# Performance work log

Measured on AMD Instinct MI355X. Metric: run time of the kernel, lower is better.

The kernel has to match this reference:

```python
import jax, jax.numpy as jnp
import numpy as np

D_MODEL = 512
NHEAD = 8
HEAD_DIM = D_MODEL // NHEAD


def setup_inputs() -> dict:
    key = jax.random.key(0)
    ks = jax.random.split(key, 12)
    B, T = 2, 4096
    inp = {
        'query': jax.random.normal(ks[0], (B, T, D_MODEL), jnp.float32),
        'key': jax.random.normal(ks[1], (B, T, D_MODEL), jnp.float32),
        'value': jax.random.normal(ks[2], (B, T, D_MODEL), jnp.float32),
        'frac': jax.random.uniform(ks[3], (B, T), jnp.float32),
        # learned parameters (torch nn.Linear: y = x @ W.T + b)
        'Wq': jax.random.normal(ks[4], (D_MODEL, D_MODEL), jnp.float32) * (D_MODEL ** -0.5),
        'bq': jnp.zeros((D_MODEL,), jnp.float32),
        'Wk': jax.random.normal(ks[5], (D_MODEL, D_MODEL), jnp.float32) * (D_MODEL ** -0.5),
        'bk': jnp.zeros((D_MODEL,), jnp.float32),
        'Wv': jax.random.normal(ks[6], (D_MODEL, D_MODEL), jnp.float32) * (D_MODEL ** -0.5),
        'bv': jnp.zeros((D_MODEL,), jnp.float32),
        'Wo': jax.random.normal(ks[7], (D_MODEL, D_MODEL), jnp.float32) * (D_MODEL ** -0.5),
        'bo': jnp.zeros((D_MODEL,), jnp.float32),
        'alpha_pos': jax.random.normal(ks[8], (NHEAD,), jnp.float32) * 0.1,
        'alpha_neg': jax.random.normal(ks[9], (NHEAD,), jnp.float32) * 0.1,
    }
    return inp


def reference(query, key, value, frac, Wq, bq, Wk, bk, Wv, bv, Wo, bo, alpha_pos, alpha_neg):
    B, T, _ = query.shape
    scale = HEAD_DIM ** -0.5
    # projections (torch Linear convention: x @ W.T + b)
    Q = (query @ Wq.T + bq).reshape(B, T, NHEAD, HEAD_DIM).transpose(0, 2, 1, 3)
    K = (key @ Wk.T + bk).reshape(B, T, NHEAD, HEAD_DIM).transpose(0, 2, 1, 3)
    V = (value @ Wv.T + bv).reshape(B, T, NHEAD, HEAD_DIM).transpose(0, 2, 1, 3)
    scores = jnp.einsum('bhqd,bhkd->bhqk', Q, K) * scale  # [B,H,T,T]
    # stoichiometric bias: D[b,i,j] = frac[b,j] - frac[b,i]
    D = frac[:, None, :] - frac[:, :, None]  # [B,T,T]
    D_pos = jnp.maximum(D, 0.0)
    D_neg = jnp.minimum(D, 0.0)
    bias = (alpha_pos[None, :, None, None] * D_pos[:, None]
            + alpha_neg[None, :, None, None] * D_neg[:, None])  # [B,H,T,T]
    probs = jax.nn.softmax(scores + bias, axis=-1)
    out = jnp.einsum('bhqk,bhkd->bhqd', probs, V)
    out = out.transpose(0, 2, 1, 3).reshape(B, T, D_MODEL)
    return out @ Wo.T + bo
```

## Files before the change

### kernel.cpp

```cpp
#include <hip/hip_runtime.h>

typedef __attribute__((ext_vector_type(8))) __bf16 bf16x8;
typedef __attribute__((ext_vector_type(8))) unsigned short ushort8;
typedef __attribute__((ext_vector_type(4))) float f32x4;
typedef unsigned short ushort_t;

#define MFMA_BF16(A,B,C) __builtin_amdgcn_mfma_f32_16x16x32_bf16(A,B,C,0,0,0)

#define T_SEQ 4096
#define DM 512
#define HD_ 64
#define NH_ 8

#define LOG2E 1.4426950408889634f
#define QSCALE (0.125f * LOG2E)

__device__ __forceinline__ unsigned short f2b(float f){
    unsigned int u = __builtin_bit_cast(unsigned int, f);
    u += 0x7FFFu + ((u >> 16) & 1u);
    return (unsigned short)(u >> 16);
}

__device__ __forceinline__ float exp2_fast(float x){
#if __has_builtin(__builtin_amdgcn_exp2f)
    return __builtin_amdgcn_exp2f(x);
#else
    float r; asm("v_exp_f32 %0, %1" : "=v"(r) : "v"(x)); return r;
#endif
}

__device__ __forceinline__ unsigned cvt_pk_bf16(float a, float b){
    unsigned r;
    asm("v_cvt_pk_bf16_f32 %0, %1, %2" : "=v"(r) : "v"(a), "v"(b));
    return r;
}

__device__ __forceinline__ void gload_lds16(const void* g, void* l){
    __builtin_amdgcn_global_load_lds((const __attribute__((address_space(1))) void*)g,
                                     (__attribute__((address_space(3))) void*)l, 16, 0, 0);
}

template<int OUT_BF16>
__device__ __forceinline__ void gemm_body(const float* __restrict__ A, const float* __restrict__ W,
                                          const float* __restrict__ bias, void* __restrict__ Cout,
                                          int m0, int n0, float scale)
{
    constexpr int K = 512, N = 512;
    __shared__ ushort_t As[128*64];
    __shared__ ushort_t Bs[128*64];

    const int tid  = threadIdx.x;
    const int lane = tid & 63;
    const int w    = tid >> 6;
    const int g    = lane >> 4;
    const int c16  = lane & 15;
    const int wm   = w >> 1, wn = w & 1;

    f32x4 acc[4][4];
#pragma unroll
    for (int i=0;i<4;i++)
#pragma unroll
        for (int j=0;j<4;j++) acc[i][j] = (f32x4){0.f,0.f,0.f,0.f};

#pragma unroll 1
    for (int kt=0; kt<K/64; kt++){
        __syncthreads();
#pragma unroll
        for (int j=0;j<4;j++){
            int cid = j*256 + tid;
            int row = cid >> 3, ch = cid & 7;
            const float* srcA = A + (size_t)(m0+row)*K + kt*64 + ch*8;
            const float* srcB = W + (size_t)(n0+row)*K + kt*64 + ch*8;
            float4 a0 = *(const float4*)srcA;
            float4 a1 = *(const float4*)(srcA+4);
            float4 b0 = *(const float4*)srcB;
            float4 b1 = *(const float4*)(srcB+4);
            ushort8 va, vb;
            va[0]=f2b(a0.x); va[1]=f2b(a0.y); va[2]=f2b(a0.z); va[3]=f2b(a0.w);
            va[4]=f2b(a1.x); va[5]=f2b(a1.y); va[6]=f2b(a1.z); va[7]=f2b(a1.w);
            vb[0]=f2b(b0.x); vb[1]=f2b(b0.y); vb[2]=f2b(b0.z); vb[3]=f2b(b0.w);
            vb[4]=f2b(b1.x); vb[5]=f2b(b1.y); vb[6]=f2b(b1.z); vb[7]=f2b(b1.w);
            int dst = row*64 + ((ch ^ (row & 7))<<3);
            *(ushort8*)&As[dst] = va;
            *(ushort8*)&Bs[dst] = vb;
        }
        __syncthreads();
#pragma unroll
        for (int ks=0; ks<2; ks++){
            bf16x8 af[4], bfr[4];
#pragma unroll
            for (int f=0; f<4; f++){
                int rowa = wm*64 + f*16 + c16;
                af[f]  = *(const bf16x8*)&As[rowa*64 + (((ks*4+g) ^ (rowa&7))<<3)];
                int rowb = wn*64 + f*16 + c16;
                bfr[f] = *(const bf16x8*)&Bs[rowb*64 + (((ks*4+g) ^ (rowb&7))<<3)];
            }
#pragma unroll
            for (int fm=0; fm<4; fm++)
#pragma unroll
                for (int fn=0; fn<4; fn++)
                    acc[fm][fn] = MFMA_BF16(af[fm], bfr[fn], acc[fm][fn]);
        }
    }
#pragma unroll
    for (int fm=0; fm<4; fm++)
#pragma unroll
        for (int fn=0; fn<4; fn++){
            int col = n0 + wn*64 + fn*16 + c16;
            float bv = bias[col];
#pragma unroll
            for (int r=0; r<4; r++){
                int rowm = m0 + wm*64 + fm*16 + g*4 + r;
                float vv = (acc[fm][fn][r] + bv) * scale;
                if (OUT_BF16) ((ushort_t*)Cout)[(size_t)rowm*N + col] = f2b(vv);
                else          ((float*)Cout)[(size_t)rowm*N + col]   = vv;
            }
        }
}

__global__ __launch_bounds__(256,2) void gemm_qkv_kernel(
    const float* __restrict__ q, const float* __restrict__ k, const float* __restrict__ v,
    const float* __restrict__ Wq, const float* __restrict__ bq,
    const float* __restrict__ Wk, const float* __restrict__ bk,
    const float* __restrict__ Wv, const float* __restrict__ bv,
    ushort_t* __restrict__ QKVp)
{
    int z = blockIdx.z;
    const float* A  = (z==0) ? q  : (z==1 ? k  : v);
    const float* W  = (z==0) ? Wq : (z==1 ? Wk : Wv);
    const float* bb = (z==0) ? bq : (z==1 ? bk : bv);
    float scale = (z==0) ? QSCALE : 1.0f;
    ushort_t* C = QKVp + (size_t)z * (size_t)(2*T_SEQ) * DM;
    gemm_body<1>(A, W, bb, C, blockIdx.x*128, blockIdx.y*128, scale);
}

__global__ __launch_bounds__(256,2) void gemm_out_kernel(
    const float* __restrict__ O, const float* __restrict__ Wo,
    const float* __restrict__ bo, float* __restrict__ out)
{
    gemm_body<0>(O, Wo, bo, out, blockIdx.x*128, blockIdx.y*128, 1.0f);
}

__global__ __launch_bounds__(256) void vtrans_kernel(const ushort_t* __restrict__ Vp,
                                                     ushort_t* __restrict__ Vt)
{
    int blk = blockIdx.x;
    int bh  = blk >> 6;
    int t0  = (blk & 63) << 6;
    int b = bh >> 3, h = bh & 7;
    __shared__ ushort_t tile[64][65];
    const int tid = threadIdx.x;
    const ushort_t* src = Vp + (size_t)(b*T_SEQ + t0)*DM + h*HD_;
#pragma unroll
    for (int p=0; p<2; p++){
        int row = (tid>>3) + p*32;
        int c8  = (tid&7)*8;
        ushort8 v = *(const ushort8*)(src + (size_t)row*DM + c8);
#pragma unroll
        for (int j=0;j<8;j++) tile[row][c8+j] = v[j];
    }
    __syncthreads();
    ushort_t* dst = Vt + (size_t)bh*HD_*T_SEQ + t0;
#pragma unroll
    for (int p=0; p<2; p++){
        int d  = (tid>>3) + p*32;
        int c8 = (tid&7)*8;
        ushort8 v;
#pragma unroll
        for (int j=0;j<8;j++) v[j] = tile[c8+j][d];
        *(ushort8*)(dst + (size_t)d*T_SEQ + c8) = v;
    }
}

__global__ __launch_bounds__(512,4) void flash_kernel(
    const ushort_t* __restrict__ Qp, const ushort_t* __restrict__ Kp, const ushort_t* __restrict__ Vt,
    const float* __restrict__ frac, const float* __restrict__ alphap, const float* __restrict__ alphan,
    float* __restrict__ O)
{
    int i    = blockIdx.x;
    int slot = i & 7;
    int seq  = i >> 3;
    int bh   = slot*2 + (seq >> 5);
    int qt   = seq & 31;
    int b    = bh >> 3, h = bh & 7;
    int q0   = qt * 128;

    const int tid  = threadIdx.x;
    const int w    = tid >> 6;
    const int lane = tid & 63;
    const int g    = lane >> 4;
    const int c16  = lane & 15;

    __shared__ ushort_t Ks [2][64*64];
    __shared__ ushort_t VTs[2][64*64];
    __shared__ ushort_t PW [8][16*64];

    const ushort_t* Qbase = Qp + (size_t)(b*T_SEQ)*DM + h*HD_;
    const ushort_t* Kbase = Kp + (size_t)(b*T_SEQ)*DM + h*HD_;
    const ushort_t* Vtb   = Vt + (size_t)bh*HD_*T_SEQ;
    const float*    fr    = frac + b*T_SEQ;
    const float c1 = 0.5f*(alphap[h] + alphan[h]) * LOG2E;
    const float c2 = 0.5f*(alphap[h] - alphan[h]) * LOG2E;
    const int qrow = q0 + w*16;

    bf16x8 qa[2];
#pragma unroll
    for (int ks=0; ks<2; ks++)
        qa[ks] = *(const bf16x8*)(Qbase + (size_t)(qrow + c16)*DM + ks*32 + g*8);
    const float fi = fr[qrow + c16];

    float m2   = -1e30f;
    float lsum = 0.f;
    f32x4 acc[4];
#pragma unroll
    for (int dt=0; dt<4; dt++) acc[dt] = (f32x4){0.f,0.f,0.f,0.f};

    bf16x8 vbp[2][4];

#define STAGE(BUF, KV0)                                                          \
    {                                                                            \
        int cb  = w*64;                                                          \
        int idx = cb + lane;                                                     \
        int row = idx >> 3, cc = idx & 7;                                        \
        int cs  = cc ^ (row & 7);                                                \
        gload_lds16(Kbase + (size_t)((KV0)+row)*DM + cs*8, &Ks[BUF][cb*8]);      \
        gload_lds16(Vtb + (size_t)row*T_SEQ + (KV0) + cs*8, &VTs[BUF][cb*8]);    \
    }

    STAGE(0, 0);
    asm volatile("s_waitcnt vmcnt(0)" ::: "memory");
    __syncthreads();

    int buf = 0;
#pragma unroll 1
    for (int kt=0; kt<T_SEQ/64; kt++){
        int kv0 = kt*64;
        if (kt+1 < T_SEQ/64) STAGE(buf^1, kv0+64);

        bf16x8 pb0, pb1;
        if (kt > 0){
            pb0 = *(const bf16x8*)&PW[w][c16*64 + (((    g) ^ (c16&7))<<3)];
            pb1 = *(const bf16x8*)&PW[w][c16*64 + (((4 + g) ^ (c16&7))<<3)];
        }

        f32x4 s[4];
#pragma unroll
        for (int n=0; n<4; n++) s[n] = (f32x4){0.f,0.f,0.f,0.f};
        __builtin_amdgcn_s_setprio(1);
#pragma unroll
        for (int n=0; n<4; n++){
#pragma unroll
            for (int ks=0; ks<2; ks++){
                int row = n*16 + c16;
                bf16x8 kb = *(const bf16x8*)&Ks[buf][row*64 + (((ks*4+g) ^ (row&7))<<3)];
                s[n] = MFMA_BF16(kb, qa[ks], s[n]);
            }
        }
        if (kt > 0){
#pragma unroll
            for (int dt=0; dt<4; dt++) acc[dt] = MFMA_BF16(vbp[0][dt], pb0, acc[dt]);
#pragma unroll
            for (int dt=0; dt<4; dt++) acc[dt] = MFMA_BF16(vbp[1][dt], pb1, acc[dt]);
        }
        __builtin_amdgcn_s_setprio(0);
        __builtin_amdgcn_sched_barrier(0);

        float mx;
#pragma unroll
        for (int n=0; n<4; n++){
            f32x4 fj = *(const f32x4*)&fr[kv0 + n*16 + g*4];
#pragma unroll
            for (int r=0; r<4; r++){
                float dd = fj[r] - fi;
                s[n][r] = fmaf(c1, dd, fmaf(c2, fabsf(dd), s[n][r]));
            }
            float t = fmaxf(fmaxf(s[n][0], s[n][1]), fmaxf(s[n][2], s[n][3]));
            mx = (n==0) ? t : fmaxf(mx, t);
        }
        mx = fmaxf(mx, __shfl_xor(mx, 16));
        mx = fmaxf(mx, __shfl_xor(mx, 32));

        if (__any(mx > m2 + 12.0f)){
            float mnew = fmaxf(m2, mx);
            float fac  = exp2_fast(m2 - mnew);
            lsum *= fac;
#pragma unroll
            for (int dt=0; dt<4; dt++)
#pragma unroll
                for (int r=0; r<4; r++) acc[dt][r] *= fac;
            m2 = mnew;
        }

        float tn[4];
#pragma unroll
        for (int n=0; n<4; n++){
#pragma unroll
            for (int r=0; r<4; r++) s[n][r] = exp2_fast(s[n][r] - m2);
            tn[n] = (s[n][0] + s[n][1]) + (s[n][2] + s[n][3]);
            unsigned pk0 = cvt_pk_bf16(s[n][0], s[n][1]);
            unsigned pk1 = cvt_pk_bf16(s[n][2], s[n][3]);
            uint2 u; u.x = pk0; u.y = pk1;
            int off = c16*64 + (((n*2 + (g>>1)) ^ (c16 & 7))<<3) + ((g&1)<<2);
            *(uint2*)&PW[w][off] = u;
        }
        float rs = (tn[0] + tn[1]) + (tn[2] + tn[3]);
        rs += __shfl_xor(rs, 16);
        rs += __shfl_xor(rs, 32);
        lsum += rs;

#pragma unroll
        for (int ks=0; ks<2; ks++)
#pragma unroll
            for (int dt=0; dt<4; dt++){
                int vr = dt*16 + c16;
                vbp[ks][dt] = *(const bf16x8*)&VTs[buf][vr*64 + (((ks*4+g) ^ (vr&7))<<3)];
            }

        asm volatile("s_waitcnt vmcnt(0)" ::: "memory");
        __syncthreads();
        buf ^= 1;
    }
#undef STAGE

    {
        bf16x8 pb0 = *(const bf16x8*)&PW[w][c16*64 + (((    g) ^ (c16&7))<<3)];
        bf16x8 pb1 = *(const bf16x8*)&PW[w][c16*64 + (((4 + g) ^ (c16&7))<<3)];
#pragma unroll
        for (int dt=0; dt<4; dt++) acc[dt] = MFMA_BF16(vbp[0][dt], pb0, acc[dt]);
#pragma unroll
        for (int dt=0; dt<4; dt++) acc[dt] = MFMA_BF16(vbp[1][dt], pb1, acc[dt]);
    }

    float inv = 1.0f / lsum;
    float* orow = O + (size_t)(b*T_SEQ + qrow + c16)*DM + h*HD_;
#pragma unroll
    for (int dt=0; dt<4; dt++){
        float4 o4;
        o4.x = acc[dt][0]*inv; o4.y = acc[dt][1]*inv;
        o4.z = acc[dt][2]*inv; o4.w = acc[dt][3]*inv;
        *(float4*)(orow + dt*16 + g*4) = o4;
    }
}

extern "C" void kernel_launch(void* const* d_in, const int* in_sizes, int n_in,
                              void* d_out, int out_size, void* d_ws, size_t ws_size,
                              hipStream_t stream)
{
    const float* q  = (const float*)d_in[0];
    const float* k  = (const float*)d_in[1];
    const float* v  = (const float*)d_in[2];
    const float* fr = (const float*)d_in[3];
    const float* Wq = (const float*)d_in[4];
    const float* bq = (const float*)d_in[5];
    const float* Wk = (const float*)d_in[6];
    const float* bk = (const float*)d_in[7];
    const float* Wv = (const float*)d_in[8];
    const float* bv = (const float*)d_in[9];
    const float* Wo = (const float*)d_in[10];
    const float* bo = (const float*)d_in[11];
    const float* ap = (const float*)d_in[12];
    const float* an = (const float*)d_in[13];

    const size_t MT = (size_t)(2*T_SEQ) * DM;
    ushort_t* QKVp = (ushort_t*)d_ws;
    ushort_t* Vtp  = QKVp + 3*MT;
    float*    O    = (float*)((char*)d_ws + 4*MT*sizeof(ushort_t));

    dim3 gq(64, 4, 3);
    gemm_qkv_kernel<<<gq, 256, 0, stream>>>(q,k,v,Wq,bq,Wk,bk,Wv,bv,QKVp);

    vtrans_kernel<<<1024, 256, 0, stream>>>(QKVp + 2*MT, Vtp);

    flash_kernel<<<512, 512, 0, stream>>>(QKVp, QKVp + MT, Vtp, fr, ap, an, O);

    dim3 go(64, 4, 1);
    gemm_out_kernel<<<go, 256, 0, stream>>>(O, Wo, bo, (float*)d_out);
}
```

Measured before the change: 171.6 us.

## Fuse V transpose into QKV GEMM epilogue and compute row sums via MFMA

The V projection GEMM now writes its output directly in the head-major transposed layout, which removes the separate transpose kernel launch and its extra global read and write of V. Inside the flash kernel, the softmax row sum is accumulated with an extra MFMA against a vector of bf16 ones, replacing the VALU additions and cross-lane shuffle reduction. The row max is computed with a flatter tree of three-input max operations. The trade-offs are uncoalesced 8-byte scattered stores in the V epilogue and a row sum built from bf16-rounded probabilities, which can differ slightly from the fp32 sum.

```diff
diff --git a/kernel.cpp b/kernel.cpp
--- a/kernel.cpp
+++ b/kernel.cpp
@@ -2,6 +2,7 @@
 
 typedef __attribute__((ext_vector_type(8))) __bf16 bf16x8;
 typedef __attribute__((ext_vector_type(8))) unsigned short ushort8;
+typedef __attribute__((ext_vector_type(4))) unsigned short ushort4_t;
 typedef __attribute__((ext_vector_type(4))) float f32x4;
 typedef unsigned short ushort_t;
 
@@ -29,6 +30,10 @@
 #endif
 }
 
+__device__ __forceinline__ float max3f(float a, float b, float c){
+    return fmaxf(fmaxf(a, b), c);
+}
+
 __device__ __forceinline__ unsigned cvt_pk_bf16(float a, float b){
     unsigned r;
     asm("v_cvt_pk_bf16_f32 %0, %1, %2" : "=v"(r) : "v"(a), "v"(b));
@@ -40,7 +45,7 @@
                                      (__attribute__((address_space(3))) void*)l, 16, 0, 0);
 }
 
-template<int OUT_BF16>
+template<int MODE>
 __device__ __forceinline__ void gemm_body(const float* __restrict__ A, const float* __restrict__ W,
                                           const float* __restrict__ bias, void* __restrict__ Cout,
                                           int m0, int n0, float scale)
@@ -108,12 +113,24 @@
         for (int fn=0; fn<4; fn++){
             int col = n0 + wn*64 + fn*16 + c16;
             float bv = bias[col];
-#pragma unroll
-            for (int r=0; r<4; r++){
-                int rowm = m0 + wm*64 + fm*16 + g*4 + r;
-                float vv = (acc[fm][fn][r] + bv) * scale;
-                if (OUT_BF16) ((ushort_t*)Cout)[(size_t)rowm*N + col] = f2b(vv);
-                else          ((float*)Cout)[(size_t)rowm*N + col]   = vv;
+            if (MODE == 2){
+                int t0r = m0 + wm*64 + fm*16 + g*4;
+                int b2  = t0r >> 12;
+                int t   = t0r & 4095;
+                int h2  = col >> 6, d = col & 63;
+                ushort4_t u;
+#pragma unroll
+                for (int r=0; r<4; r++) u[r] = f2b(acc[fm][fn][r] + bv);
+                ushort_t* dst = (ushort_t*)Cout + ((size_t)(b2*NH_ + h2)*HD_ + d)*T_SEQ + t;
+                *(ushort4_t*)dst = u;
+            } else {
+#pragma unroll
+                for (int r=0; r<4; r++){
+                    int rowm = m0 + wm*64 + fm*16 + g*4 + r;
+                    float vv = (acc[fm][fn][r] + bv) * scale;
+                    if (MODE == 1) ((ushort_t*)Cout)[(size_t)rowm*N + col] = f2b(vv);
+                    else           ((float*)Cout)[(size_t)rowm*N + col]   = vv;
+                }
             }
         }
 }
@@ -129,9 +146,12 @@
     const float* A  = (z==0) ? q  : (z==1 ? k  : v);
     const float* W  = (z==0) ? Wq : (z==1 ? Wk : Wv);
     const float* bb = (z==0) ? bq : (z==1 ? bk : bv);
-    float scale = (z==0) ? QSCALE : 1.0f;
     ushort_t* C = QKVp + (size_t)z * (size_t)(2*T_SEQ) * DM;
-    gemm_body<1>(A, W, bb, C, blockIdx.x*128, blockIdx.y*128, scale);
+    if (z == 2)
+        gemm_body<2>(A, W, bb, C, blockIdx.x*128, blockIdx.y*128, 1.0f);
+    else
+        gemm_body<1>(A, W, bb, C, blockIdx.x*128, blockIdx.y*128,
+                     (z==0) ? QSCALE : 1.0f);
 }
 
 __global__ __launch_bounds__(256,2) void gemm_out_kernel(
@@ -139,37 +159,6 @@
     const float* __restrict__ bo, float* __restrict__ out)
 {
     gemm_body<0>(O, Wo, bo, out, blockIdx.x*128, blockIdx.y*128, 1.0f);
-}
-
-__global__ __launch_bounds__(256) void vtrans_kernel(const ushort_t* __restrict__ Vp,
-                                                     ushort_t* __restrict__ Vt)
-{
-    int blk = blockIdx.x;
-    int bh  = blk >> 6;
-    int t0  = (blk & 63) << 6;
-    int b = bh >> 3, h = bh & 7;
-    __shared__ ushort_t tile[64][65];
-    const int tid = threadIdx.x;
-    const ushort_t* src = Vp + (size_t)(b*T_SEQ + t0)*DM + h*HD_;
-#pragma unroll
-    for (int p=0; p<2; p++){
-        int row = (tid>>3) + p*32;
-        int c8  = (tid&7)*8;
-        ushort8 v = *(const ushort8*)(src + (size_t)row*DM + c8);
-#pragma unroll
-        for (int j=0;j<8;j++) tile[row][c8+j] = v[j];
-    }
-    __syncthreads();
-    ushort_t* dst = Vt + (size_t)bh*HD_*T_SEQ + t0;
-#pragma unroll
-    for (int p=0; p<2; p++){
-        int d  = (tid>>3) + p*32;
-        int c8 = (tid&7)*8;
-        ushort8 v;
-#pragma unroll
-        for (int j=0;j<8;j++) v[j] = tile[c8+j][d];
-        *(ushort8*)(dst + (size_t)d*T_SEQ + c8) = v;
-    }
 }
 
 __global__ __launch_bounds__(512,4) void flash_kernel(
@@ -209,11 +198,17 @@
         qa[ks] = *(const bf16x8*)(Qbase + (size_t)(qrow + c16)*DM + ks*32 + g*8);
     const float fi = fr[qrow + c16];
 
-    float m2   = -1e30f;
-    float lsum = 0.f;
+    ushort8 ou;
+#pragma unroll
+    for (int j=0;j<8;j++) ou[j] = 0x3F80;
+    const bf16x8 ones = __builtin_bit_cast(bf16x8, ou);
+
+    float m2 = -1e30f;
     f32x4 acc[4];
+    f32x4 asum;
 #pragma unroll
     for (int dt=0; dt<4; dt++) acc[dt] = (f32x4){0.f,0.f,0.f,0.f};
+    asum = (f32x4){0.f,0.f,0.f,0.f};
 
     bf16x8 vbp[2][4];
 
@@ -257,15 +252,16 @@
             }
         }
         if (kt > 0){
+            asum = MFMA_BF16(ones, pb0, asum);
 #pragma unroll
             for (int dt=0; dt<4; dt++) acc[dt] = MFMA_BF16(vbp[0][dt], pb0, acc[dt]);
+            asum = MFMA_BF16(ones, pb1, asum);
 #pragma unroll
             for (int dt=0; dt<4; dt++) acc[dt] = MFMA_BF16(vbp[1][dt], pb1, acc[dt]);
         }
         __builtin_amdgcn_s_setprio(0);
         __builtin_amdgcn_sched_barrier(0);
 
-        float mx;
 #pragma unroll
         for (int n=0; n<4; n++){
             f32x4 fj = *(const f32x4*)&fr[kv0 + n*16 + g*4];
@@ -274,8 +270,15 @@
                 float dd = fj[r] - fi;
                 s[n][r] = fmaf(c1, dd, fmaf(c2, fabsf(dd), s[n][r]));
             }
-            float t = fmaxf(fmaxf(s[n][0], s[n][1]), fmaxf(s[n][2], s[n][3]));
-            mx = (n==0) ? t : fmaxf(mx, t);
+        }
+        float mx;
+        {
+            float t0 = max3f(s[0][0], s[0][1], s[0][2]);
+            float t1 = max3f(s[0][3], s[1][0], s[1][1]);
+            float t2 = max3f(s[1][2], s[1][3], s[2][0]);
+            float t3 = max3f(s[2][1], s[2][2], s[2][3]);
+            float t4 = max3f(s[3][0], s[3][1], s[3][2]);
+            mx = fmaxf(max3f(t0, t1, t2), max3f(t3, t4, s[3][3]));
         }
         mx = fmaxf(mx, __shfl_xor(mx, 16));
         mx = fmaxf(mx, __shfl_xor(mx, 32));
@@ -283,7 +286,8 @@
         if (__any(mx > m2 + 12.0f)){
             float mnew = fmaxf(m2, mx);
             float fac  = exp2_fast(m2 - mnew);
-            lsum *= fac;
+#pragma unroll
+            for (int r=0; r<4; r++) asum[r] *= fac;
 #pragma unroll
             for (int dt=0; dt<4; dt++)
 #pragma unroll
@@ -291,22 +295,16 @@
             m2 = mnew;
         }
 
-        float tn[4];
 #pragma unroll
         for (int n=0; n<4; n++){
 #pragma unroll
             for (int r=0; r<4; r++) s[n][r] = exp2_fast(s[n][r] - m2);
-            tn[n] = (s[n][0] + s[n][1]) + (s[n][2] + s[n][3]);
             unsigned pk0 = cvt_pk_bf16(s[n][0], s[n][1]);
             unsigned pk1 = cvt_pk_bf16(s[n][2], s[n][3]);
             uint2 u; u.x = pk0; u.y = pk1;
             int off = c16*64 + (((n*2 + (g>>1)) ^ (c16 & 7))<<3) + ((g&1)<<2);
             *(uint2*)&PW[w][off] = u;
         }
-        float rs = (tn[0] + tn[1]) + (tn[2] + tn[3]);
-        rs += __shfl_xor(rs, 16);
-        rs += __shfl_xor(rs, 32);
-        lsum += rs;
 
 #pragma unroll
         for (int ks=0; ks<2; ks++)
@@ -325,13 +323,15 @@
     {
         bf16x8 pb0 = *(const bf16x8*)&PW[w][c16*64 + (((    g) ^ (c16&7))<<3)];
         bf16x8 pb1 = *(const bf16x8*)&PW[w][c16*64 + (((4 + g) ^ (c16&7))<<3)];
+        asum = MFMA_BF16(ones, pb0, asum);
 #pragma unroll
         for (int dt=0; dt<4; dt++) acc[dt] = MFMA_BF16(vbp[0][dt], pb0, acc[dt]);
+        asum = MFMA_BF16(ones, pb1, asum);
 #pragma unroll
         for (int dt=0; dt<4; dt++) acc[dt] = MFMA_BF16(vbp[1][dt], pb1, acc[dt]);
     }
 
-    float inv = 1.0f / lsum;
+    float inv = 1.0f / asum[0];
     float* orow = O + (size_t)(b*T_SEQ + qrow + c16)*DM + h*HD_;
 #pragma unroll
     for (int dt=0; dt<4; dt++){
@@ -363,15 +363,12 @@
 
     const size_t MT = (size_t)(2*T_SEQ) * DM;
     ushort_t* QKVp = (ushort_t*)d_ws;
-    ushort_t* Vtp  = QKVp + 3*MT;
-    float*    O    = (float*)((char*)d_ws + 4*MT*sizeof(ushort_t));
+    float*    O    = (float*)((char*)d_ws + 3*MT*sizeof(ushort_t));
 
     dim3 gq(64, 4, 3);
     gemm_qkv_kernel<<<gq, 256, 0, stream>>>(q,k,v,Wq,bq,Wk,bk,Wv,bv,QKVp);
 
-    vtrans_kernel<<<1024, 256, 0, stream>>>(QKVp + 2*MT, Vtp);
-
-    flash_kernel<<<512, 512, 0, stream>>>(QKVp, QKVp + MT, Vtp, fr, ap, an, O);
+    flash_kernel<<<512, 512, 0, stream>>>(QKVp, QKVp + MT, QKVp + 2*MT, fr, ap, an, O);
 
     dim3 go(64, 4, 1);
     gemm_out_kernel<<<go, 256, 0, stream>>>(O, Wo, bo, (float*)d_out);
```

After: 167.0 us (median of 3 runs). -2.7%, faster.
